# Optimization experiments

Measured on AMD Instinct MI355X. Metric: run time of the kernel, lower is better.

## Reference

```python
import jax, jax.numpy as jnp
import numpy as np


def conv1x1(x, W, b):
    # 1x1 Conv2d == per-pixel linear over channels. x: [B,C,H,W], W: [O,C], b: [O]
    return jnp.einsum('oc,bchw->bohw', W, x) + b[None, :, None, None]


def setup_inputs() -> dict:
    key = jax.random.key(0)
    ks = jax.random.split(key, 18)
    B, C, Hd, H, W = 16, 64, 64, 32, 32
    s = 0.05
    f = jax.random.normal
    return {
        'h': f(ks[0], (B, C, H, W), jnp.float32),
        'm': f(ks[1], (B, C, H, W), jnp.float32),
        'Wq': f(ks[2], (Hd, C), jnp.float32) * s,
        'bq': f(ks[3], (Hd,), jnp.float32) * s,
        'Wk': f(ks[4], (Hd, C), jnp.float32) * s,
        'bk': f(ks[5], (Hd,), jnp.float32) * s,
        'Wk2': f(ks[6], (Hd, C), jnp.float32) * s,
        'bk2': f(ks[7], (Hd,), jnp.float32) * s,
        'Wv': f(ks[8], (C, C), jnp.float32) * s,
        'bv': f(ks[9], (C,), jnp.float32) * s,
        'Wv2': f(ks[10], (C, C), jnp.float32) * s,
        'bv2': f(ks[11], (C,), jnp.float32) * s,
        'Wz': f(ks[12], (2 * C, 2 * C), jnp.float32) * s,
        'bz': f(ks[13], (2 * C,), jnp.float32) * s,
        'Wm': f(ks[14], (3 * C, 3 * C), jnp.float32) * s,
        'bm': f(ks[15], (3 * C,), jnp.float32) * s,
    }


def reference(h, m, Wq, bq, Wk, bk, Wk2, bk2, Wv, bv, Wv2, bv2, Wz, bz, Wm, bm):
    B, C, H, W = h.shape
    Hd = Wq.shape[0]
    N = H * W
    # Shared query from h
    Q_h = conv1x1(h, Wq, bq).reshape(B, Hd, N).transpose(0, 2, 1)  # [B,N,Hd]
    # Self-attention branch over h
    K_h = conv1x1(h, Wk, bk).reshape(B, Hd, N)                     # [B,Hd,N]
    A_h = jax.nn.softmax(jnp.einsum('bnd,bdm->bnm', Q_h, K_h), axis=-1)  # [B,N,N]
    V_h = conv1x1(h, Wv, bv).reshape(B, C, N)                      # [B,C,N]
    Z_h = jnp.einsum('bnm,bcm->bcn', A_h, V_h).reshape(B, C, H, W)
    # Cross-attention branch over memory m (same query Q_h)
    K_m = conv1x1(m, Wk2, bk2).reshape(B, Hd, N)
    A_m = jax.nn.softmax(jnp.einsum('bnd,bdm->bnm', Q_h, K_m), axis=-1)
    V_m = conv1x1(m, Wv2, bv2).reshape(B, C, N)
    Z_m = jnp.einsum('bnm,bcm->bcn', A_m, V_m).reshape(B, C, H, W)
    # Fuse and gated memory update
    Z = conv1x1(jnp.concatenate([Z_h, Z_m], axis=1), Wz, bz)       # [B,2C,H,W]
    combined = conv1x1(jnp.concatenate([Z, h], axis=1), Wm, bm)    # [B,3C,H,W]
    mo, mg, mi = combined[:, :C], combined[:, C:2 * C], combined[:, 2 * C:]
    mi = jax.nn.sigmoid(mi)
    new_m = (1 - mi) * m + mi * jnp.tanh(mg)
    new_h = jax.nn.sigmoid(mo) * new_m
    return (new_h, new_m)
```

## Files before the change

### kernel.cpp

```cpp
#include <hip/hip_runtime.h>

typedef unsigned short u16;
typedef unsigned int u32;
typedef __attribute__((ext_vector_type(8))) short bf16x8;
typedef __attribute__((ext_vector_type(4))) short bf16x4;
typedef __attribute__((ext_vector_type(4))) float f32x4;

#define MFMA(a, b, c) __builtin_amdgcn_mfma_f32_16x16x32_bf16((a), (b), (c), 0, 0, 0)
#define MFMA16(a, b, c) __builtin_amdgcn_mfma_f32_16x16x16bf16_1k((a), (b), (c), 0, 0, 0)

static __device__ __forceinline__ u16 f2bf(float x) {
  u32 u = __float_as_uint(x);
  u += 0x7FFFu + ((u >> 16) & 1u);
  return (u16)(u >> 16);
}
static __device__ __forceinline__ u32 packbf_t(float hi, float lo) {
  return __builtin_amdgcn_perm(__float_as_uint(hi), __float_as_uint(lo), 0x07060302u);
}
static __device__ __forceinline__ u32 packbf(float lo, float hi) {
  return (u32)f2bf(lo) | ((u32)f2bf(hi) << 16);
}
static __device__ __forceinline__ bf16x8 ld8bf(const float* __restrict__ p) {
  const float4 a = *(const float4*)p;
  const float4 b = *(const float4*)(p + 4);
  union { u32 u[4]; bf16x8 v; } r;
  r.u[0] = packbf(a.x, a.y);
  r.u[1] = packbf(a.z, a.w);
  r.u[2] = packbf(b.x, b.y);
  r.u[3] = packbf(b.z, b.w);
  return r.v;
}

__global__ __launch_bounds__(256, 2) void fused_attn_kernel(
    const float* __restrict__ h, const float* __restrict__ m_,
    const float* __restrict__ Wq, const float* __restrict__ bq,
    const float* __restrict__ Wk, const float* __restrict__ bk,
    const float* __restrict__ Wk2, const float* __restrict__ bk2,
    const float* __restrict__ Wv, const float* __restrict__ bv,
    const float* __restrict__ Wv2, const float* __restrict__ bv2,
    u16* __restrict__ hbuf, u16* __restrict__ Ztb)
{
  const int id = blockIdx.x;
  const int b = id & 15;
  const int br = (id >> 4) & 1;
  const int qh = id >> 5;
  const float* __restrict__ X = (br ? m_ : h) + b * 65536;
  const float* __restrict__ H = h + b * 65536;
  const float* __restrict__ WK = br ? Wk2 : Wk;
  const float* __restrict__ BK = br ? bk2 : bk;
  const float* __restrict__ WV = br ? Wv2 : Wv;
  const float* __restrict__ BV = br ? bv2 : bv;

  __shared__ __align__(16) u16 Qlds[64 * 72];
  __shared__ __align__(16) u16 Klds[64 * 72];
  __shared__ __align__(16) u16 zcb[4 * 64 * 68];
  __shared__ float rsw[4][64];

  const int tid = threadIdx.x, w = tid >> 6, lane = tid & 63;
  const int mm = lane & 15, q = lane >> 4;
  const int q0 = qh * 64;

  bf16x8 wqA0[4], wqA1[4], wkA0[4], wkA1[4], wvB0[4], wvB1[4];
#pragma unroll
  for (int ot = 0; ot < 4; ++ot) {
    const int ro = (ot * 16 + mm) * 64;
    wqA0[ot] = ld8bf(Wq + ro + q * 8);
    wqA1[ot] = ld8bf(Wq + ro + 32 + q * 8);
    wkA0[ot] = ld8bf(WK + ro + q * 8);
    wkA1[ot] = ld8bf(WK + ro + 32 + q * 8);
    wvB0[ot] = ld8bf(WV + ro + q * 8);
    wvB1[ot] = ld8bf(WV + ro + 32 + q * 8);
  }
  float4 bkq[4];
  float bvs[4];
#pragma unroll
  for (int ot = 0; ot < 4; ++ot) {
    bkq[ot] = *(const float4*)(BK + ot * 16 + q * 4);
    bvs[ot] = BV[ot * 16 + mm];
  }

  {
    const int qp = q0 + w * 16 + mm;
    float xq[16];
#pragma unroll
    for (int i = 0; i < 2; ++i)
#pragma unroll
      for (int j = 0; j < 8; ++j) xq[i * 8 + j] = H[(i * 32 + q * 8 + j) * 1024 + qp];
    union { u32 u[4]; bf16x8 v; } x0, x1;
#pragma unroll
    for (int p = 0; p < 4; ++p) {
      x0.u[p] = packbf(xq[2 * p], xq[2 * p + 1]);
      x1.u[p] = packbf(xq[8 + 2 * p], xq[9 + 2 * p]);
    }
    if (br == 0) {
      u16* hp = hbuf + (b * 1024 + qp) * 64;
      uint4 h0, h1;
      h0.x = x0.u[0]; h0.y = x0.u[1]; h0.z = x0.u[2]; h0.w = x0.u[3];
      h1.x = x1.u[0]; h1.y = x1.u[1]; h1.z = x1.u[2]; h1.w = x1.u[3];
      *(uint4*)(hp + q * 8) = h0;
      *(uint4*)(hp + 32 + q * 8) = h1;
    }
#pragma unroll
    for (int ot = 0; ot < 4; ++ot) {
      const float4 b4 = *(const float4*)(bq + ot * 16 + q * 4);
      f32x4 d = {b4.x, b4.y, b4.z, b4.w};
      d = MFMA(wqA0[ot], x0.v, d);
      d = MFMA(wqA1[ot], x1.v, d);
      uint2 val;
      val.x = packbf(d[0], d[1]);
      val.y = packbf(d[2], d[3]);
      *(uint2*)(Qlds + (w * 16 + mm) * 72 + ot * 16 + q * 4) = val;
    }
  }
  __syncthreads();
  bf16x8 qb0[4], qb1[4];
#pragma unroll
  for (int qt = 0; qt < 4; ++qt) {
    qb0[qt] = *(const bf16x8*)(Qlds + (qt * 16 + mm) * 72 + q * 8);
    qb1[qt] = *(const bf16x8*)(Qlds + (qt * 16 + mm) * 72 + 32 + q * 8);
  }

  f32x4 z[4][4];
#pragma unroll
  for (int qt = 0; qt < 4; ++qt)
#pragma unroll
    for (int ct = 0; ct < 4; ++ct) z[qt][ct] = (f32x4){0.f, 0.f, 0.f, 0.f};
  float rp[4] = {0.f, 0.f, 0.f, 0.f};

  float xn[16];
  union { u32 u[4]; bf16x8 v; } xb0, xb1;
  auto xload = [&](int kc) {
    const float* Xp = X + kc * 64 + w * 16 + mm;
#pragma unroll
    for (int i = 0; i < 2; ++i)
#pragma unroll
      for (int j = 0; j < 8; ++j) xn[i * 8 + j] = Xp[(i * 32 + q * 8 + j) * 1024];
  };
  auto xpack = [&]() {
#pragma unroll
    for (int p = 0; p < 4; ++p) {
      xb0.u[p] = packbf(xn[2 * p], xn[2 * p + 1]);
      xb1.u[p] = packbf(xn[8 + 2 * p], xn[9 + 2 * p]);
    }
  };

  xload(0);
  xpack();
#pragma unroll 1
  for (int kc = 0; kc < 16; ++kc) {
    if (kc < 15) xload(kc + 1);

#pragma unroll
    for (int ot = 0; ot < 4; ++ot) {
      f32x4 d = {bkq[ot].x, bkq[ot].y, bkq[ot].z, bkq[ot].w};
      d = MFMA(wkA0[ot], xb0.v, d);
      d = MFMA(wkA1[ot], xb1.v, d);
      uint2 val;
      val.x = packbf(d[0], d[1]);
      val.y = packbf(d[2], d[3]);
      *(uint2*)(Klds + (w * 16 + mm) * 72 + ot * 16 + q * 4) = val;
    }
    const bf16x8 kf0 = *(const bf16x8*)(Klds + (w * 16 + mm) * 72 + q * 8);
    const bf16x8 kf1 = *(const bf16x8*)(Klds + (w * 16 + mm) * 72 + 32 + q * 8);

    bf16x4 vf[4];
#pragma unroll
    for (int ct = 0; ct < 4; ++ct) {
      f32x4 d = {bvs[ct], bvs[ct], bvs[ct], bvs[ct]};
      d = MFMA(xb0.v, wvB0[ct], d);
      d = MFMA(xb1.v, wvB1[ct], d);
      union { u32 u[2]; bf16x4 v; } pv;
      pv.u[0] = packbf_t(d[1], d[0]);
      pv.u[1] = packbf_t(d[3], d[2]);
      vf[ct] = pv.v;
    }

#pragma unroll
    for (int qt = 0; qt < 4; ++qt) {
      f32x4 s = {0.f, 0.f, 0.f, 0.f};
      s = MFMA(kf0, qb0[qt], s);
      s = MFMA(kf1, qb1[qt], s);
      const float e0 = __expf(s[0]), e1 = __expf(s[1]);
      const float e2 = __expf(s[2]), e3 = __expf(s[3]);
      rp[qt] += (e0 + e1) + (e2 + e3);
      union { u32 u[2]; bf16x4 v; } pb;
      pb.u[0] = packbf_t(e1, e0);
      pb.u[1] = packbf_t(e3, e2);
#pragma unroll
      for (int ct = 0; ct < 4; ++ct) z[qt][ct] = MFMA16(vf[ct], pb.v, z[qt][ct]);
    }

    if (kc < 15) xpack();
  }

#pragma unroll
  for (int qt = 0; qt < 4; ++qt) {
    float v = rp[qt];
    v += __shfl_xor(v, 16);
    v += __shfl_xor(v, 32);
    if (q == 0) rsw[w][qt * 16 + mm] = v;
#pragma unroll
    for (int ct = 0; ct < 4; ++ct) {
      uint2 val;
      val.x = packbf_t(z[qt][ct][1], z[qt][ct][0]);
      val.y = packbf_t(z[qt][ct][3], z[qt][ct][2]);
      *(uint2*)(zcb + w * 4352 + (qt * 16 + mm) * 68 + ct * 16 + q * 4) = val;
    }
  }
  __syncthreads();

  const int c2 = tid & 31, qr = tid >> 5;
#pragma unroll
  for (int i = 0; i < 8; ++i) {
    const int query = qr + i * 8;
    const float rt = rsw[0][query] + rsw[1][query] + rsw[2][query] + rsw[3][query];
    const float rinv = __builtin_amdgcn_rcpf(rt);
    float vlo = 0.f, vhi = 0.f;
#pragma unroll
    for (int ww = 0; ww < 4; ++ww) {
      const u32 u = *(const u32*)(zcb + ww * 4352 + query * 68 + c2 * 2);
      vlo += __uint_as_float(u << 16);
      vhi += __uint_as_float(u & 0xffff0000u);
    }
    vlo *= rinv;
    vhi *= rinv;
    *(u32*)(Ztb + (b * 1024 + q0 + query) * 128 + br * 64 + c2 * 2) = packbf_t(vhi, vlo);
  }
}

__global__ __launch_bounds__(256) void tail_kernel(
    const u16* __restrict__ Ztb, const u16* __restrict__ hbuf,
    const float* __restrict__ m_, const float* __restrict__ Wz,
    const float* __restrict__ bz, const float* __restrict__ Wm,
    const float* __restrict__ bm, float* __restrict__ out)
{
  const int b = blockIdx.x, n0 = blockIdx.y * 32;
  __shared__ __align__(16) u16 zp[32][136];
  const int tid = threadIdx.x, lane = tid & 63, wv = tid >> 6;
  const int mm = lane & 15, q = lane >> 4;
  const int pxt = wv & 1, oh = wv >> 1;

  {
    bf16x8 za[4];
#pragma unroll
    for (int ks = 0; ks < 4; ++ks)
      za[ks] = *(const bf16x8*)(Ztb + (b * 1024 + n0 + pxt * 16 + mm) * 128 +
                                ks * 32 + q * 8);
#pragma unroll
    for (int ot = 0; ot < 4; ++ot) {
      const int o0 = oh * 64 + ot * 16;
      const float4 b4 = *(const float4*)(bz + o0 + q * 4);
      f32x4 d = {b4.x, b4.y, b4.z, b4.w};
#pragma unroll
      for (int ks = 0; ks < 4; ++ks) {
        const bf16x8 wb = ld8bf(Wz + (o0 + mm) * 128 + ks * 32 + q * 8);
        d = MFMA(wb, za[ks], d);
      }
      uint2 val;
      val.x = packbf(d[0], d[1]);
      val.y = packbf(d[2], d[3]);
      *(uint2*)&zp[pxt * 16 + mm][o0 + q * 4] = val;
    }
  }
  __syncthreads();

  {
    const int hb2 = oh;
    bf16x8 fa[6];
#pragma unroll
    for (int ks = 0; ks < 4; ++ks)
      fa[ks] = *(const bf16x8*)&zp[pxt * 16 + mm][ks * 32 + q * 8];
    {
      const u16* hp = hbuf + (b * 1024 + n0 + pxt * 16 + mm) * 64;
      fa[4] = *(const bf16x8*)(hp + q * 8);
      fa[5] = *(const bf16x8*)(hp + 32 + q * 8);
    }
    f32x4 dd[6];
#pragma unroll
    for (int j = 0; j < 6; ++j) {
      const int o = (j % 3) * 64 + (hb2 * 2 + j / 3) * 16 + mm;
      const float bb = bm[o];
      f32x4 d = {bb, bb, bb, bb};
#pragma unroll
      for (int ks = 0; ks < 6; ++ks) {
        const bf16x8 wb = ld8bf(Wm + o * 192 + ks * 32 + q * 8);
        d = MFMA(fa[ks], wb, d);
      }
      dd[j] = d;
    }
#pragma unroll
    for (int ctl = 0; ctl < 2; ++ctl) {
      const int c = (hb2 * 2 + ctl) * 16 + mm;
      const int px = n0 + pxt * 16 + q * 4;
      const float4 mold = *(const float4*)(m_ + (b * 64 + c) * 1024 + px);
      float4 nh, nm;
#pragma unroll
      for (int r = 0; r < 4; ++r) {
        const float xo = dd[0 + ctl * 3 / 3 * 0 + (ctl * 3 + 0)][r];
        const float xg = dd[ctl * 3 + 1][r];
        const float xi = dd[ctl * 3 + 2][r];
        const float si = __builtin_amdgcn_rcpf(1.f + __expf(-xi));
        const float th = 1.f - 2.f * __builtin_amdgcn_rcpf(__expf(2.f * xg) + 1.f);
        const float so = __builtin_amdgcn_rcpf(1.f + __expf(-xo));
        const float mo = ((const float*)&mold)[r];
        const float nmv = (1.f - si) * mo + si * th;
        ((float*)&nm)[r] = nmv;
        ((float*)&nh)[r] = so * nmv;
      }
      *(float4*)(out + (b * 64 + c) * 1024 + px) = nh;
      *(float4*)(out + 1048576 + (b * 64 + c) * 1024 + px) = nm;
    }
  }
}

extern "C" void kernel_launch(void* const* d_in, const int* in_sizes, int n_in,
                              void* d_out, int out_size, void* d_ws, size_t ws_size,
                              hipStream_t stream) {
  const float* h   = (const float*)d_in[0];
  const float* m   = (const float*)d_in[1];
  const float* Wq  = (const float*)d_in[2];
  const float* bq  = (const float*)d_in[3];
  const float* Wk  = (const float*)d_in[4];
  const float* bk  = (const float*)d_in[5];
  const float* Wk2 = (const float*)d_in[6];
  const float* bk2 = (const float*)d_in[7];
  const float* Wv  = (const float*)d_in[8];
  const float* bv  = (const float*)d_in[9];
  const float* Wv2 = (const float*)d_in[10];
  const float* bv2 = (const float*)d_in[11];
  const float* Wz  = (const float*)d_in[12];
  const float* bz  = (const float*)d_in[13];
  const float* Wm  = (const float*)d_in[14];
  const float* bm  = (const float*)d_in[15];
  float* out = (float*)d_out;

  char* ws = (char*)d_ws;
  const size_t MB = 1024 * 1024;
  u16* hbuf = (u16*)(ws + 0 * MB);
  u16* Ztb  = (u16*)(ws + 2 * MB);

  fused_attn_kernel<<<512, 256, 0, stream>>>(h, m, Wq, bq, Wk, bk, Wk2, bk2,
                                             Wv, bv, Wv2, bv2, hbuf, Ztb);
  tail_kernel<<<dim3(16, 32), 256, 0, stream>>>(Ztb, hbuf, m, Wz, bz, Wm, bm, out);
}
```

Before: 156.8 us.

## Fold key projection into query via Q·Wk and halve query tile per block

Scores are computed as X·(Wk^T Q) + Q·bk, so the key conv is no longer evaluated for every key chunk; a per-query projected vector QW is built once and multiplied directly against raw input pixels. The query tile shrinks from 64 to 32, which doubles the grid and lets the kernel declare four blocks per CU, with LDS pooled and reused for the Z reduction. This removes the per-chunk K MFMAs and LDS round trip but recomputes the V projection per block over twice as many blocks, and it drops the register prefetch of the next X chunk. Rounding QW to bf16 also changes numerics slightly.

```diff
diff --git a/kernel.cpp b/kernel.cpp
--- a/kernel.cpp
+++ b/kernel.cpp
@@ -31,7 +31,7 @@
   return r.v;
 }
 
-__global__ __launch_bounds__(256, 2) void fused_attn_kernel(
+__global__ __launch_bounds__(256, 4) void fused_attn_kernel(
     const float* __restrict__ h, const float* __restrict__ m_,
     const float* __restrict__ Wq, const float* __restrict__ bq,
     const float* __restrict__ Wk, const float* __restrict__ bk,
@@ -51,41 +51,34 @@
   const float* __restrict__ WV = br ? Wv2 : Wv;
   const float* __restrict__ BV = br ? bv2 : bv;
 
-  __shared__ __align__(16) u16 Qlds[64 * 72];
-  __shared__ __align__(16) u16 Klds[64 * 72];
-  __shared__ __align__(16) u16 zcb[4 * 64 * 68];
-  __shared__ float rsw[4][64];
+  __shared__ __align__(16) u16 pool[8704];
+  __shared__ float rsw[4][32];
+  __shared__ float cql[32];
+  u16* const Qlds = pool;
+  u16* const QWlds = pool + 2304;
+  u16* const zcb = pool;
 
   const int tid = threadIdx.x, w = tid >> 6, lane = tid & 63;
   const int mm = lane & 15, q = lane >> 4;
-  const int q0 = qh * 64;
-
-  bf16x8 wqA0[4], wqA1[4], wkA0[4], wkA1[4], wvB0[4], wvB1[4];
+  const int q0 = qh * 32;
+
+  bf16x8 wvB0[4], wvB1[4];
+  float bvs[4];
 #pragma unroll
   for (int ot = 0; ot < 4; ++ot) {
-    const int ro = (ot * 16 + mm) * 64;
-    wqA0[ot] = ld8bf(Wq + ro + q * 8);
-    wqA1[ot] = ld8bf(Wq + ro + 32 + q * 8);
-    wkA0[ot] = ld8bf(WK + ro + q * 8);
-    wkA1[ot] = ld8bf(WK + ro + 32 + q * 8);
-    wvB0[ot] = ld8bf(WV + ro + q * 8);
-    wvB1[ot] = ld8bf(WV + ro + 32 + q * 8);
-  }
-  float4 bkq[4];
-  float bvs[4];
-#pragma unroll
-  for (int ot = 0; ot < 4; ++ot) {
-    bkq[ot] = *(const float4*)(BK + ot * 16 + q * 4);
+    wvB0[ot] = ld8bf(WV + (ot * 16 + mm) * 64 + q * 8);
+    wvB1[ot] = ld8bf(WV + (ot * 16 + mm) * 64 + 32 + q * 8);
     bvs[ot] = BV[ot * 16 + mm];
   }
 
-  {
+  if (w < 2) {
     const int qp = q0 + w * 16 + mm;
     float xq[16];
 #pragma unroll
     for (int i = 0; i < 2; ++i)
 #pragma unroll
-      for (int j = 0; j < 8; ++j) xq[i * 8 + j] = H[(i * 32 + q * 8 + j) * 1024 + qp];
+      for (int j = 0; j < 8; ++j)
+        xq[i * 8 + j] = H[(i * 32 + q * 8 + j) * 1024 + qp];
     union { u32 u[4]; bf16x8 v; } x0, x1;
 #pragma unroll
     for (int p = 0; p < 4; ++p) {
@@ -100,68 +93,83 @@
       *(uint4*)(hp + q * 8) = h0;
       *(uint4*)(hp + 32 + q * 8) = h1;
     }
+    float cqp = 0.f;
 #pragma unroll
     for (int ot = 0; ot < 4; ++ot) {
+      const bf16x8 wa0 = ld8bf(Wq + (ot * 16 + mm) * 64 + q * 8);
+      const bf16x8 wa1 = ld8bf(Wq + (ot * 16 + mm) * 64 + 32 + q * 8);
       const float4 b4 = *(const float4*)(bq + ot * 16 + q * 4);
       f32x4 d = {b4.x, b4.y, b4.z, b4.w};
-      d = MFMA(wqA0[ot], x0.v, d);
-      d = MFMA(wqA1[ot], x1.v, d);
+      d = MFMA(wa0, x0.v, d);
+      d = MFMA(wa1, x1.v, d);
+      const float4 bkv = *(const float4*)(BK + ot * 16 + q * 4);
+      cqp += d[0] * bkv.x + d[1] * bkv.y + d[2] * bkv.z + d[3] * bkv.w;
       uint2 val;
       val.x = packbf(d[0], d[1]);
       val.y = packbf(d[2], d[3]);
       *(uint2*)(Qlds + (w * 16 + mm) * 72 + ot * 16 + q * 4) = val;
     }
-  }
-  __syncthreads();
-  bf16x8 qb0[4], qb1[4];
-#pragma unroll
-  for (int qt = 0; qt < 4; ++qt) {
-    qb0[qt] = *(const bf16x8*)(Qlds + (qt * 16 + mm) * 72 + q * 8);
-    qb1[qt] = *(const bf16x8*)(Qlds + (qt * 16 + mm) * 72 + 32 + q * 8);
-  }
-
-  f32x4 z[4][4];
-#pragma unroll
-  for (int qt = 0; qt < 4; ++qt)
-#pragma unroll
-    for (int ct = 0; ct < 4; ++ct) z[qt][ct] = (f32x4){0.f, 0.f, 0.f, 0.f};
-  float rp[4] = {0.f, 0.f, 0.f, 0.f};
-
-  float xn[16];
-  union { u32 u[4]; bf16x8 v; } xb0, xb1;
-  auto xload = [&](int kc) {
-    const float* Xp = X + kc * 64 + w * 16 + mm;
-#pragma unroll
-    for (int i = 0; i < 2; ++i)
-#pragma unroll
-      for (int j = 0; j < 8; ++j) xn[i * 8 + j] = Xp[(i * 32 + q * 8 + j) * 1024];
-  };
-  auto xpack = [&]() {
-#pragma unroll
-    for (int p = 0; p < 4; ++p) {
-      xb0.u[p] = packbf(xn[2 * p], xn[2 * p + 1]);
-      xb1.u[p] = packbf(xn[8 + 2 * p], xn[9 + 2 * p]);
-    }
-  };
-
-  xload(0);
-  xpack();
-#pragma unroll 1
-  for (int kc = 0; kc < 16; ++kc) {
-    if (kc < 15) xload(kc + 1);
-
-#pragma unroll
-    for (int ot = 0; ot < 4; ++ot) {
-      f32x4 d = {bkq[ot].x, bkq[ot].y, bkq[ot].z, bkq[ot].w};
-      d = MFMA(wkA0[ot], xb0.v, d);
-      d = MFMA(wkA1[ot], xb1.v, d);
+    cqp += __shfl_xor(cqp, 16);
+    cqp += __shfl_xor(cqp, 32);
+    if (q == 0) cql[w * 16 + mm] = cqp;
+  }
+  __syncthreads();
+
+  if (w < 2) {
+    const bf16x8 qB0 = *(const bf16x8*)(Qlds + (w * 16 + mm) * 72 + q * 8);
+    const bf16x8 qB1 = *(const bf16x8*)(Qlds + (w * 16 + mm) * 72 + 32 + q * 8);
+#pragma unroll
+    for (int ct2 = 0; ct2 < 4; ++ct2) {
+      union { u32 u[4]; bf16x8 v; } a0, a1;
+#pragma unroll
+      for (int jp = 0; jp < 4; ++jp) {
+        const float w00 = WK[(q * 8 + 2 * jp) * 64 + ct2 * 16 + mm];
+        const float w01 = WK[(q * 8 + 2 * jp + 1) * 64 + ct2 * 16 + mm];
+        const float w10 = WK[(32 + q * 8 + 2 * jp) * 64 + ct2 * 16 + mm];
+        const float w11 = WK[(32 + q * 8 + 2 * jp + 1) * 64 + ct2 * 16 + mm];
+        a0.u[jp] = packbf(w00, w01);
+        a1.u[jp] = packbf(w10, w11);
+      }
+      f32x4 d = {0.f, 0.f, 0.f, 0.f};
+      d = MFMA(a0.v, qB0, d);
+      d = MFMA(a1.v, qB1, d);
       uint2 val;
       val.x = packbf(d[0], d[1]);
       val.y = packbf(d[2], d[3]);
-      *(uint2*)(Klds + (w * 16 + mm) * 72 + ot * 16 + q * 4) = val;
-    }
-    const bf16x8 kf0 = *(const bf16x8*)(Klds + (w * 16 + mm) * 72 + q * 8);
-    const bf16x8 kf1 = *(const bf16x8*)(Klds + (w * 16 + mm) * 72 + 32 + q * 8);
+      *(uint2*)(QWlds + (w * 16 + mm) * 72 + ct2 * 16 + q * 4) = val;
+    }
+  }
+  __syncthreads();
+
+  bf16x8 qwf0[2], qwf1[2];
+  float cq2[2];
+#pragma unroll
+  for (int qt = 0; qt < 2; ++qt) {
+    qwf0[qt] = *(const bf16x8*)(QWlds + (qt * 16 + mm) * 72 + q * 8);
+    qwf1[qt] = *(const bf16x8*)(QWlds + (qt * 16 + mm) * 72 + 32 + q * 8);
+    cq2[qt] = cql[qt * 16 + mm];
+  }
+
+  f32x4 z[2][4];
+#pragma unroll
+  for (int qt = 0; qt < 2; ++qt)
+#pragma unroll
+    for (int ct = 0; ct < 4; ++ct) z[qt][ct] = (f32x4){0.f, 0.f, 0.f, 0.f};
+  float rp[2] = {0.f, 0.f};
+
+#pragma unroll 1
+  for (int kc = 0; kc < 16; ++kc) {
+    const int px = w * 256 + kc * 16 + mm;
+    union { u32 u[4]; bf16x8 v; } xb0, xb1;
+#pragma unroll
+    for (int jp = 0; jp < 4; ++jp) {
+      const float f00 = X[(q * 8 + 2 * jp) * 1024 + px];
+      const float f01 = X[(q * 8 + 2 * jp + 1) * 1024 + px];
+      const float f10 = X[(32 + q * 8 + 2 * jp) * 1024 + px];
+      const float f11 = X[(32 + q * 8 + 2 * jp + 1) * 1024 + px];
+      xb0.u[jp] = packbf(f00, f01);
+      xb1.u[jp] = packbf(f10, f11);
+    }
 
     bf16x4 vf[4];
 #pragma unroll
@@ -176,10 +184,10 @@
     }
 
 #pragma unroll
-    for (int qt = 0; qt < 4; ++qt) {
-      f32x4 s = {0.f, 0.f, 0.f, 0.f};
-      s = MFMA(kf0, qb0[qt], s);
-      s = MFMA(kf1, qb1[qt], s);
+    for (int qt = 0; qt < 2; ++qt) {
+      f32x4 s = {cq2[qt], cq2[qt], cq2[qt], cq2[qt]};
+      s = MFMA(xb0.v, qwf0[qt], s);
+      s = MFMA(xb1.v, qwf1[qt], s);
       const float e0 = __expf(s[0]), e1 = __expf(s[1]);
       const float e2 = __expf(s[2]), e3 = __expf(s[3]);
       rp[qt] += (e0 + e1) + (e2 + e3);
@@ -189,12 +197,12 @@
 #pragma unroll
       for (int ct = 0; ct < 4; ++ct) z[qt][ct] = MFMA16(vf[ct], pb.v, z[qt][ct]);
     }
-
-    if (kc < 15) xpack();
-  }
-
-#pragma unroll
-  for (int qt = 0; qt < 4; ++qt) {
+  }
+
+  __syncthreads();
+
+#pragma unroll
+  for (int qt = 0; qt < 2; ++qt) {
     float v = rp[qt];
     v += __shfl_xor(v, 16);
     v += __shfl_xor(v, 32);
@@ -204,21 +212,21 @@
       uint2 val;
       val.x = packbf_t(z[qt][ct][1], z[qt][ct][0]);
       val.y = packbf_t(z[qt][ct][3], z[qt][ct][2]);
-      *(uint2*)(zcb + w * 4352 + (qt * 16 + mm) * 68 + ct * 16 + q * 4) = val;
+      *(uint2*)(zcb + w * 2176 + (qt * 16 + mm) * 68 + ct * 16 + q * 4) = val;
     }
   }
   __syncthreads();
 
   const int c2 = tid & 31, qr = tid >> 5;
 #pragma unroll
-  for (int i = 0; i < 8; ++i) {
+  for (int i = 0; i < 4; ++i) {
     const int query = qr + i * 8;
     const float rt = rsw[0][query] + rsw[1][query] + rsw[2][query] + rsw[3][query];
     const float rinv = __builtin_amdgcn_rcpf(rt);
     float vlo = 0.f, vhi = 0.f;
 #pragma unroll
     for (int ww = 0; ww < 4; ++ww) {
-      const u32 u = *(const u32*)(zcb + ww * 4352 + query * 68 + c2 * 2);
+      const u32 u = *(const u32*)(zcb + ww * 2176 + query * 68 + c2 * 2);
       vlo += __uint_as_float(u << 16);
       vhi += __uint_as_float(u & 0xffff0000u);
     }
@@ -296,7 +304,7 @@
       float4 nh, nm;
 #pragma unroll
       for (int r = 0; r < 4; ++r) {
-        const float xo = dd[0 + ctl * 3 / 3 * 0 + (ctl * 3 + 0)][r];
+        const float xo = dd[ctl * 3 + 0][r];
         const float xg = dd[ctl * 3 + 1][r];
         const float xi = dd[ctl * 3 + 2][r];
         const float si = __builtin_amdgcn_rcpf(1.f + __expf(-xi));
@@ -339,7 +347,7 @@
   u16* hbuf = (u16*)(ws + 0 * MB);
   u16* Ztb  = (u16*)(ws + 2 * MB);
 
-  fused_attn_kernel<<<512, 256, 0, stream>>>(h, m, Wq, bq, Wk, bk, Wk2, bk2,
-                                             Wv, bv, Wv2, bv2, hbuf, Ztb);
+  fused_attn_kernel<<<1024, 256, 0, stream>>>(h, m, Wq, bq, Wk, bk, Wk2, bk2,
+                                              Wv, bv, Wv2, bv2, hbuf, Ztb);
   tail_kernel<<<dim3(16, 32), 256, 0, stream>>>(Ztb, hbuf, m, Wz, bz, Wm, bm, out);
 }
```

New measurement: 218.1 us. 39.1% more time.
